# Optimization experiments

Measured on AMD Instinct MI355X. Metric: run time of the kernel, lower is better.

Reference implementation:

```python
import jax, jax.numpy as jnp
import numpy as np

MULTI_INFER_NUM = 8
D_EMBED = 128
T, B = 256, 32


def setup_inputs() -> dict:
    key = jax.random.key(0)
    k1, k2, k3, k4 = jax.random.split(key, 4)
    positions = jax.random.randint(k1, (T, B), 0, 12, dtype=jnp.int64)
    outputs = jax.random.normal(k2, (T, B, D_EMBED), dtype=jnp.float32)
    W = jax.random.normal(k3, (MULTI_INFER_NUM + 1, D_EMBED, D_EMBED), dtype=jnp.float32)
    b = jax.random.normal(k4, (MULTI_INFER_NUM + 1, D_EMBED), dtype=jnp.float32)
    return {"positions": positions, "outputs": outputs, "W": W, "b": b}


def reference(positions, outputs, W, b):
    # Clamp positions >= multi_infer_num to the last (overflow) expert slot.
    r_pos = jnp.where(positions < MULTI_INFER_NUM, positions, MULTI_INFER_NUM)  # [T,B]
    # Gather per-token d x d transfer matrix, then batched matvec + bias,
    # matching tf.nn.embedding_lookup + einsum('ibde,ibd->ibe').
    w_gathered = W[r_pos]                         # [T,B,d,d]
    y = jnp.einsum('tbde,tbd->tbe', w_gathered, outputs)
    y = y + b[r_pos]                              # [T,B,d]
    return y
```

## Files before the change

### kernel.cpp

```cpp
#include <hip/hip_runtime.h>
#include <cstdint>

#define D 128
#define NEXP 9
#define TPB 256
#define CH0 512
#define CH8 128

typedef __bf16 bf16x8_t __attribute__((ext_vector_type(8)));
typedef float  f32x4_t  __attribute__((ext_vector_type(4)));

union FragA { uint32_t u[4]; bf16x8_t v; };

__device__ __forceinline__ uint32_t pack2_bf16(float a, float b) {
    uint32_t ua = __builtin_bit_cast(uint32_t, a);
    uint32_t ub = __builtin_bit_cast(uint32_t, b);
    ua += 0x7fffu + ((ua >> 16) & 1u);
    ub += 0x7fffu + ((ub >> 16) & 1u);
    return (ua >> 16) | (ub & 0xffff0000u);
}

__global__ __launch_bounds__(TPB) void ltf_kernel(
    const int* __restrict__ pos, const float* __restrict__ x,
    const float* __restrict__ W, const float* __restrict__ bias,
    float* __restrict__ y, int ntok, int c0)
{
    __shared__ uint32_t Wf[8192];
    __shared__ int lst[CH0];
    __shared__ int cnt;

    const int tid  = threadIdx.x;
    const int lane = tid & 63;
    const int wv   = tid >> 6;
    const int bid  = blockIdx.x;

    int r, start, C;
    if (bid < 8 * c0) { r = bid / c0; start = (bid - r * c0) * CH0; C = CH0; }
    else              { r = 8; start = (bid - 8 * c0) * CH8; C = CH8; }

    if (tid == 0) cnt = 0;
    __syncthreads();

    const int end = (start + C < ntok) ? start + C : ntok;
    #pragma unroll
    for (int it = 0; it < CH0 / TPB; ++it) {
        int t = start + it * TPB + tid;
        bool m = false;
        if (t < end) {
            int p = pos[t];
            int rp = p < (NEXP - 1) ? p : (NEXP - 1);
            m = (rp == r);
        }
        unsigned long long mask = __ballot(m);
        int nm = __popcll(mask);
        int base = 0;
        if (lane == 0 && nm > 0) base = atomicAdd(&cnt, nm);
        base = __shfl(base, 0);
        if (m) {
            int pre = __popcll(mask & ((1ull << lane) - 1ull));
            lst[base + pre] = t;
        }
    }

    const float* Wr = W + (size_t)r * D * D;
    #pragma unroll
    for (int i = 0; i < 8; ++i) {
        int s = i * TPB + tid;
        int l = s & 63, T = s >> 6;
        int q = l >> 4, m = l & 15;
        int kt = T >> 3, n = T & 7;
        const float* src = Wr + (kt * 32 + q * 8) * D + n * 16 + m;
        uint32_t u0 = pack2_bf16(src[0 * D], src[1 * D]);
        uint32_t u1 = pack2_bf16(src[2 * D], src[3 * D]);
        uint32_t u2 = pack2_bf16(src[4 * D], src[5 * D]);
        uint32_t u3 = pack2_bf16(src[6 * D], src[7 * D]);
        *reinterpret_cast<uint4*>(&Wf[s * 4]) = uint4{u0, u1, u2, u3};
    }
    __syncthreads();

    const int nc = cnt;
    const int q = lane >> 4, mloc = lane & 15;

    float bvn[8];
    #pragma unroll
    for (int n = 0; n < 8; ++n) bvn[n] = bias[(size_t)r * D + n * 16 + mloc];

    const int rounds = (nc + 63) >> 6;
    for (int rd = 0; rd < rounds; ++rd) {
        const int b16 = rd * 64 + wv * 16;
        if (b16 >= nc) continue;

        int ta = b16 + mloc; if (ta >= nc) ta = nc - 1;
        const int tokA = lst[ta];
        const float4* xrow = reinterpret_cast<const float4*>(x + (size_t)tokA * D);

        f32x4_t acc[8];
        #pragma unroll
        for (int n = 0; n < 8; ++n) acc[n] = f32x4_t{0.f, 0.f, 0.f, 0.f};

        #pragma unroll
        for (int kt = 0; kt < 4; ++kt) {
            float4 va = xrow[kt * 8 + q * 2];
            float4 vb = xrow[kt * 8 + q * 2 + 1];
            FragA a;
            a.u[0] = pack2_bf16(va.x, va.y);
            a.u[1] = pack2_bf16(va.z, va.w);
            a.u[2] = pack2_bf16(vb.x, vb.y);
            a.u[3] = pack2_bf16(vb.z, vb.w);
            #pragma unroll
            for (int n = 0; n < 8; ++n) {
                bf16x8_t bf = *reinterpret_cast<const bf16x8_t*>(
                    &Wf[(kt * 8 + n) * 256 + lane * 4]);
                acc[n] = __builtin_amdgcn_mfma_f32_16x16x32_bf16(
                    a.v, bf, acc[n], 0, 0, 0);
            }
        }

        #pragma unroll
        for (int reg = 0; reg < 4; ++reg) {
            int tloc = b16 + q * 4 + reg;
            if (tloc < nc) {
                int tok = lst[tloc];
                float* yr = y + (size_t)tok * D + mloc;
                #pragma unroll
                for (int n = 0; n < 8; ++n)
                    yr[n * 16] = acc[n][reg] + bvn[n];
            }
        }
    }
}

extern "C" void kernel_launch(void* const* d_in, const int* in_sizes, int n_in,
                              void* d_out, int out_size, void* d_ws, size_t ws_size,
                              hipStream_t stream) {
    const int* pos  = (const int*)d_in[0];
    const float* x  = (const float*)d_in[1];
    const float* W  = (const float*)d_in[2];
    const float* b  = (const float*)d_in[3];
    float* y = (float*)d_out;

    const int ntok = in_sizes[0];
    const int c0 = (ntok + CH0 - 1) / CH0;
    const int c8 = (ntok + CH8 - 1) / CH8;
    ltf_kernel<<<8 * c0 + c8, TPB, 0, stream>>>(pos, x, W, b, y, ntok, c0);
}
```

Baseline: 66.95 us.

## Pre-convert W and x to bf16 in a prep kernel and async-copy W into LDS

Adds a preprocessing kernel that converts every expert's W into the MFMA-swizzled bf16 layout and converts all of x to bf16 in a workspace. The main kernel then fills LDS with global_load_lds async copies instead of doing strided fp32 loads and per-block conversion. It also uses one uniform chunk size of 256 tokens for all 9 experts instead of the separate 512 and 128 chunk sizes. This removes the W conversion that every block repeated and halves the x bytes the main kernel reads. In exchange it adds a second kernel launch plus an extra full pass that reads x and writes its bf16 copy.

```diff
diff --git a/kernel.cpp b/kernel.cpp
--- a/kernel.cpp
+++ b/kernel.cpp
@@ -4,13 +4,10 @@
 #define D 128
 #define NEXP 9
 #define TPB 256
-#define CH0 512
-#define CH8 128
+#define CH 256
 
 typedef __bf16 bf16x8_t __attribute__((ext_vector_type(8)));
 typedef float  f32x4_t  __attribute__((ext_vector_type(4)));
-
-union FragA { uint32_t u[4]; bf16x8_t v; };
 
 __device__ __forceinline__ uint32_t pack2_bf16(float a, float b) {
     uint32_t ua = __builtin_bit_cast(uint32_t, a);
@@ -20,13 +17,52 @@
     return (ua >> 16) | (ub & 0xffff0000u);
 }
 
+__device__ __forceinline__ void async_copy16(const void* g, void* l) {
+    __builtin_amdgcn_global_load_lds(
+        (const __attribute__((address_space(1))) void*)g,
+        (__attribute__((address_space(3))) void*)l,
+        16, 0, 0);
+}
+
+__global__ __launch_bounds__(TPB) void prep_kernel(
+    const float* __restrict__ W, const float* __restrict__ x,
+    uint32_t* __restrict__ WfG, uint32_t* __restrict__ xb,
+    int nWitems, int nxitems)
+{
+    int gid = blockIdx.x * TPB + threadIdx.x;
+    if (gid < nWitems) {
+        int r = gid >> 11;
+        int s = gid & 2047;
+        int l = s & 63, T = s >> 6;
+        int q = l >> 4, m = l & 15;
+        int kt = T >> 3, n = T & 7;
+        const float* src = W + ((size_t)r << 14) + (kt * 32 + q * 8) * D + n * 16 + m;
+        uint32_t u0 = pack2_bf16(src[0 * D], src[1 * D]);
+        uint32_t u1 = pack2_bf16(src[2 * D], src[3 * D]);
+        uint32_t u2 = pack2_bf16(src[4 * D], src[5 * D]);
+        uint32_t u3 = pack2_bf16(src[6 * D], src[7 * D]);
+        *reinterpret_cast<uint4*>(&WfG[(size_t)(r * 8192 + s * 4)]) = uint4{u0, u1, u2, u3};
+    } else {
+        int xi = gid - nWitems;
+        if (xi < nxitems) {
+            const float4* src = reinterpret_cast<const float4*>(x + (size_t)xi * 8);
+            float4 a = src[0], b = src[1];
+            uint32_t u0 = pack2_bf16(a.x, a.y);
+            uint32_t u1 = pack2_bf16(a.z, a.w);
+            uint32_t u2 = pack2_bf16(b.x, b.y);
+            uint32_t u3 = pack2_bf16(b.z, b.w);
+            *reinterpret_cast<uint4*>(&xb[(size_t)xi * 4]) = uint4{u0, u1, u2, u3};
+        }
+    }
+}
+
 __global__ __launch_bounds__(TPB) void ltf_kernel(
-    const int* __restrict__ pos, const float* __restrict__ x,
-    const float* __restrict__ W, const float* __restrict__ bias,
+    const int* __restrict__ pos, const uint32_t* __restrict__ WfG,
+    const __bf16* __restrict__ xb, const float* __restrict__ bias,
     float* __restrict__ y, int ntok, int c0)
 {
     __shared__ uint32_t Wf[8192];
-    __shared__ int lst[CH0];
+    __shared__ int lst[CH];
     __shared__ int cnt;
 
     const int tid  = threadIdx.x;
@@ -34,65 +70,52 @@
     const int wv   = tid >> 6;
     const int bid  = blockIdx.x;
 
-    int r, start, C;
-    if (bid < 8 * c0) { r = bid / c0; start = (bid - r * c0) * CH0; C = CH0; }
-    else              { r = 8; start = (bid - 8 * c0) * CH8; C = CH8; }
+    const int r     = bid / c0;
+    const int start = (bid - r * c0) * CH;
+    const int end   = (start + CH < ntok) ? start + CH : ntok;
+
+    const int t = start + tid;
+    int pv = 0x7fffffff;
+    if (t < end) pv = pos[t];
 
     if (tid == 0) cnt = 0;
     __syncthreads();
 
-    const int end = (start + C < ntok) ? start + C : ntok;
-    #pragma unroll
-    for (int it = 0; it < CH0 / TPB; ++it) {
-        int t = start + it * TPB + tid;
-        bool m = false;
-        if (t < end) {
-            int p = pos[t];
-            int rp = p < (NEXP - 1) ? p : (NEXP - 1);
-            m = (rp == r);
-        }
+    {
+        const uint32_t* wsrc = WfG + (size_t)r * 8192 + wv * 2048 + lane * 4;
+        uint32_t* ldst = &Wf[wv * 2048];
+        #pragma unroll
+        for (int i = 0; i < 8; ++i)
+            async_copy16(wsrc + i * 256, ldst + i * 256);
+    }
+
+    {
+        int rp = pv < (NEXP - 1) ? pv : (NEXP - 1);
+        bool m = (t < end) && (rp == r);
         unsigned long long mask = __ballot(m);
         int nm = __popcll(mask);
         int base = 0;
         if (lane == 0 && nm > 0) base = atomicAdd(&cnt, nm);
         base = __shfl(base, 0);
-        if (m) {
-            int pre = __popcll(mask & ((1ull << lane) - 1ull));
-            lst[base + pre] = t;
-        }
+        if (m) lst[base + __popcll(mask & ((1ull << lane) - 1ull))] = t;
     }
 
-    const float* Wr = W + (size_t)r * D * D;
-    #pragma unroll
-    for (int i = 0; i < 8; ++i) {
-        int s = i * TPB + tid;
-        int l = s & 63, T = s >> 6;
-        int q = l >> 4, m = l & 15;
-        int kt = T >> 3, n = T & 7;
-        const float* src = Wr + (kt * 32 + q * 8) * D + n * 16 + m;
-        uint32_t u0 = pack2_bf16(src[0 * D], src[1 * D]);
-        uint32_t u1 = pack2_bf16(src[2 * D], src[3 * D]);
-        uint32_t u2 = pack2_bf16(src[4 * D], src[5 * D]);
-        uint32_t u3 = pack2_bf16(src[6 * D], src[7 * D]);
-        *reinterpret_cast<uint4*>(&Wf[s * 4]) = uint4{u0, u1, u2, u3};
-    }
-    __syncthreads();
-
-    const int nc = cnt;
     const int q = lane >> 4, mloc = lane & 15;
 
     float bvn[8];
     #pragma unroll
     for (int n = 0; n < 8; ++n) bvn[n] = bias[(size_t)r * D + n * 16 + mloc];
 
-    const int rounds = (nc + 63) >> 6;
-    for (int rd = 0; rd < rounds; ++rd) {
+    __syncthreads();
+    const int nc = cnt;
+
+    for (int rd = 0; rd * 64 < nc; ++rd) {
         const int b16 = rd * 64 + wv * 16;
         if (b16 >= nc) continue;
 
         int ta = b16 + mloc; if (ta >= nc) ta = nc - 1;
         const int tokA = lst[ta];
-        const float4* xrow = reinterpret_cast<const float4*>(x + (size_t)tokA * D);
+        const __bf16* xrow = xb + (size_t)tokA * D;
 
         f32x4_t acc[8];
         #pragma unroll
@@ -100,19 +123,12 @@
 
         #pragma unroll
         for (int kt = 0; kt < 4; ++kt) {
-            float4 va = xrow[kt * 8 + q * 2];
-            float4 vb = xrow[kt * 8 + q * 2 + 1];
-            FragA a;
-            a.u[0] = pack2_bf16(va.x, va.y);
-            a.u[1] = pack2_bf16(va.z, va.w);
-            a.u[2] = pack2_bf16(vb.x, vb.y);
-            a.u[3] = pack2_bf16(vb.z, vb.w);
+            bf16x8_t av = *reinterpret_cast<const bf16x8_t*>(xrow + kt * 32 + q * 8);
             #pragma unroll
             for (int n = 0; n < 8; ++n) {
                 bf16x8_t bf = *reinterpret_cast<const bf16x8_t*>(
                     &Wf[(kt * 8 + n) * 256 + lane * 4]);
-                acc[n] = __builtin_amdgcn_mfma_f32_16x16x32_bf16(
-                    a.v, bf, acc[n], 0, 0, 0);
+                acc[n] = __builtin_amdgcn_mfma_f32_16x16x32_bf16(av, bf, acc[n], 0, 0, 0);
             }
         }
 
@@ -140,7 +156,16 @@
     float* y = (float*)d_out;
 
     const int ntok = in_sizes[0];
-    const int c0 = (ntok + CH0 - 1) / CH0;
-    const int c8 = (ntok + CH8 - 1) / CH8;
-    ltf_kernel<<<8 * c0 + c8, TPB, 0, stream>>>(pos, x, W, b, y, ntok, c0);
+
+    uint32_t* wsp = (uint32_t*)d_ws;
+    uint32_t* WfG = wsp;
+    uint32_t* xb  = wsp + 131072;
+
+    const int nW = NEXP * 2048;
+    const int nx = ntok * 16;
+    const int gprep = (nW + nx + TPB - 1) / TPB;
+    prep_kernel<<<gprep, TPB, 0, stream>>>(W, x, WfG, xb, nW, nx);
+
+    const int c0 = (ntok + CH - 1) / CH;
+    ltf_kernel<<<NEXP * c0, TPB, 0, stream>>>(pos, WfG, (const __bf16*)xb, b, y, ntok, c0);
 }
```

Measured after the change: 68.32 us. 1.02x slower.
